# Performance work log

Hardware: AMD Instinct MI355X
Metric: run time of the kernel (lower is better)

## Reference

```python
import jax, jax.numpy as jnp
import numpy as np

B, N, T = 64, 1024, 512  # batch, node_num (= input_dim = hidden_dim), seq_len


def setup_inputs() -> dict:
    key = jax.random.key(0)
    k0, k1, k2, k3, k4 = jax.random.split(key, 5)
    flow_x = jax.random.normal(k0, (B, N, T, 1), dtype=jnp.float32)
    s = 1.0 / np.sqrt(N)  # torch nn.Linear default init bound
    W1 = jax.random.uniform(k1, (N, 2 * N), jnp.float32, -s, s)
    b1 = jax.random.uniform(k2, (2 * N,), jnp.float32, -s, s)
    W2 = jax.random.uniform(k3, (N, N), jnp.float32, -s, s)
    b2 = jax.random.uniform(k4, (N,), jnp.float32, -s, s)
    return {"flow_x": flow_x, "W1": W1, "b1": b1, "W2": W2, "b2": b2}


def reference(flow_x, W1, b1, W2, b2):
    Bs, Nn, Ts, _ = flow_x.shape
    # [B, N, T, 1] -> [B, T, N]
    x = jnp.transpose(flow_x, (0, 2, 1, 3)).reshape(Bs, Ts, Nn)
    # Precompute input projections for all timesteps (batched GEMM)
    xp = x @ W1 + b1                      # [B, T, 2N]
    xh = x @ W2 + b2                      # [B, T, N]
    x1, x2 = jnp.split(xp, 2, axis=-1)    # each [B, T, N]

    def step(h, inp):
        x1t, x2t, xht = inp               # each [B, N]
        hp = h @ W1 + b1                  # [B, 2N]
        h1, h2 = jnp.split(hp, 2, axis=-1)
        z = jax.nn.sigmoid(x1t + h1)
        r = jax.nn.sigmoid(x2t + h2)
        h_hat = jnp.tanh(xht + r * (h @ W2 + b2))
        h_new = z * h + (1.0 - z) * h_hat
        return h_new, None

    h0 = jnp.zeros((Bs, Nn), dtype=x.dtype)
    xs = (jnp.swapaxes(x1, 0, 1), jnp.swapaxes(x2, 0, 1), jnp.swapaxes(xh, 0, 1))
    hT, _ = jax.lax.scan(step, h0, xs)
    # original returns last output reshaped to [B, N, 1, 1]
    return hT.reshape(Bs, Nn, 1, 1)
```

## Files before the change

kernel.cpp:

```cpp
#include <hip/hip_runtime.h>


#define BATCH 64
#define NN 1024
#define TSTEPS 512
#define HB_ELEMS ((size_t)BATCH * NN)
#define SPIN_CAP 16384

typedef __attribute__((ext_vector_type(8))) short short8;
typedef __attribute__((ext_vector_type(8))) unsigned short u16x8;
typedef __attribute__((ext_vector_type(4))) unsigned short u16x4;
typedef __attribute__((ext_vector_type(4))) float f32x4;

#define MFMA16(a, b, c) __builtin_amdgcn_mfma_f32_16x16x32_bf16((a), (b), (c), 0, 0, 0)

__device__ __forceinline__ unsigned short f2bf(float x) {
  union { float f; unsigned u; } v; v.f = x;
  unsigned u = v.u + 0x7FFFu + ((v.u >> 16) & 1u);
  return (unsigned short)(u >> 16);
}
__device__ __forceinline__ float bf2f(unsigned short h) {
  union { unsigned u; float f; } v; v.u = ((unsigned)h) << 16; return v.f;
}

__global__ void trans_x(const float* __restrict__ fx, unsigned short* __restrict__ xT) {
  int bid = blockIdx.x;
  int b   = bid >> 7;
  int rem = bid & 127;
  int kt  = rem >> 3;
  int tt  = rem & 7;
  __shared__ float tl[64][65];
  int tx = threadIdx.x & 63;
  int ty = threadIdx.x >> 6;
  const float* src = fx + ((size_t)(b * NN + kt * 64)) * TSTEPS + tt * 64;
#pragma unroll
  for (int i = 0; i < 16; i++) {
    int kr = i * 4 + ty;
    tl[kr][tx] = src[(size_t)kr * TSTEPS + tx];
  }
  __syncthreads();
#pragma unroll
  for (int i = 0; i < 16; i++) {
    int tr = i * 4 + ty;
    xT[((size_t)((tt * 64 + tr) * 64 + b)) * NN + kt * 64 + tx] = f2bf(tl[tx][tr]);
  }
}

__global__ void prep_w(const float* __restrict__ W1, const float* __restrict__ W2,
                       unsigned short* __restrict__ wt) {
  int bid = blockIdx.x;
  int s    = bid >> 8;
  int tile = bid & 255;
  int kt = tile >> 4, jt = tile & 15;
  const float* src = (s < 2) ? W1 : W2;
  int ld = (s < 2) ? 2048 : 1024;
  int co = (s == 1) ? 1024 : 0;
  __shared__ float tl[64][65];
  int tx = threadIdx.x & 63, ty = threadIdx.x >> 6;
#pragma unroll
  for (int i = 0; i < 16; i++) {
    int kr = i * 4 + ty;
    tl[kr][tx] = src[(size_t)(kt * 64 + kr) * ld + co + jt * 64 + tx];
  }
  __syncthreads();
#pragma unroll
  for (int i = 0; i < 16; i++) {
    int jr = i * 4 + ty;
    wt[((size_t)(s * NN + jt * 64 + jr)) * NN + kt * 64 + tx] = f2bf(tl[tx][jr]);
  }
}

__global__ __launch_bounds__(256) void precompute(
    const unsigned short* __restrict__ xT, const unsigned short* __restrict__ wt,
    const float* __restrict__ b1, const float* __restrict__ b2,
    unsigned short* __restrict__ P2) {
  int m0 = (blockIdx.x / 24) * 128;
  int n0 = (blockIdx.x % 24) * 128;
  __shared__ unsigned short As[128 * 40];
  __shared__ unsigned short Bs[128 * 40];
  int tid = threadIdx.x;
  int wave = tid >> 6, lane = tid & 63, q = lane >> 4, li = lane & 15;
  int wm = wave >> 1, wn = wave & 1;
  f32x4 acc[4][4];
#pragma unroll
  for (int a = 0; a < 4; a++)
#pragma unroll
    for (int b = 0; b < 4; b++) acc[a][b] = (f32x4)(0.f);

  for (int kk = 0; kk < 32; ++kk) {
    int K0 = kk * 32;
#pragma unroll
    for (int e = 0; e < 2; e++) {
      int c = tid * 2 + e;
      int row = c >> 2, part = c & 3;
      *(u16x8*)&As[row * 40 + part * 8] =
          *(const u16x8*)&xT[(size_t)(m0 + row) * NN + K0 + part * 8];
      *(u16x8*)&Bs[row * 40 + part * 8] =
          *(const u16x8*)&wt[(size_t)(n0 + row) * NN + K0 + part * 8];
    }
    __syncthreads();
    short8 af[4], bfr[4];
#pragma unroll
    for (int mt = 0; mt < 4; mt++)
      af[mt] = *(const short8*)&As[(wm * 64 + mt * 16 + li) * 40 + q * 8];
#pragma unroll
    for (int nt = 0; nt < 4; nt++)
      bfr[nt] = *(const short8*)&Bs[(wn * 64 + nt * 16 + li) * 40 + q * 8];
#pragma unroll
    for (int mt = 0; mt < 4; mt++)
#pragma unroll
      for (int nt = 0; nt < 4; nt++)
        acc[mt][nt] = MFMA16(af[mt], bfr[nt], acc[mt][nt]);
    __syncthreads();
  }
#pragma unroll
  for (int mt = 0; mt < 4; mt++) {
    int m = m0 + wm * 64 + mt * 16 + q * 4;
    int t = m >> 6, b = m & 63;
#pragma unroll
    for (int nt = 0; nt < 4; nt++) {
      int n = n0 + wn * 64 + nt * 16 + li;
      float bias = (n < 2048) ? b1[n] : b2[n - 2048];
      int s = n >> 10, j = n & 1023;
      f32x4 a = acc[mt][nt];
      u16x4 pk;
      pk.x = f2bf(a.x + bias); pk.y = f2bf(a.y + bias);
      pk.z = f2bf(a.z + bias); pk.w = f2bf(a.w + bias);
      *(u16x4*)&P2[(((size_t)t * 3 + s) * NN + j) * 64 + b] = pk;
    }
  }
}

#define AL(p)    __hip_atomic_load((p),  __ATOMIC_RELAXED, __HIP_MEMORY_SCOPE_AGENT)
#define AS(p, v) __hip_atomic_store((p), (v), __ATOMIC_RELAXED, __HIP_MEMORY_SCOPE_AGENT)

__global__ __launch_bounds__(256, 1) void gru_scan(
    unsigned short* __restrict__ hb, const unsigned short* __restrict__ wt,
    const unsigned short* __restrict__ P2,
    const float* __restrict__ b1, const float* __restrict__ b2,
    float* __restrict__ out, unsigned* __restrict__ flags) {
  int bid = blockIdx.x;
  int jt = bid & 63, mq = bid >> 6;
  int j0 = jt * 16, m0 = mq * 16;
  int tid = threadIdx.x, wave = tid >> 6, lane = tid & 63, q = lane >> 4, li = lane & 15;
  int kb = wave * 256;

  const short8* Bz = (const short8*)&wt[((size_t)(0 * NN + j0 + li)) * NN + kb + q * 8];
  const short8* Br = (const short8*)&wt[((size_t)(1 * NN + j0 + li)) * NN + kb + q * 8];
  const short8* Bv = (const short8*)&wt[((size_t)(2 * NN + j0 + li)) * NN + kb + q * 8];
  short8 wz[8], wr[8], wv[8];
#pragma unroll
  for (int r = 0; r < 8; r++) {
    wz[r] = Bz[r * 4];
    wr[r] = Br[r * 4];
    wv[r] = Bv[r * 4];
  }

  int j = j0 + li;
  int bbase = m0 + q * 4;
  float b1z = b1[j], b1r = b1[NN + j], b2v = b2[j];
  const unsigned short* pz = &P2[((size_t)0 * NN + j) * 64 + bbase];
  const unsigned short* pr = &P2[((size_t)1 * NN + j) * 64 + bbase];
  const unsigned short* pv = &P2[((size_t)2 * NN + j) * 64 + bbase];
  const size_t pstride = (size_t)3 * NN * 64;

  unsigned* myflag = &flags[(mq * 4 + (jt >> 4)) * 64 + (jt & 15)];
  const unsigned* pollp = &flags[(mq * 4 + wave) * 64 + li];

  const size_t aoff = (size_t)(m0 + li) * 256 + wave * 64 + q * 2;

  f32x4 hc = (f32x4)(0.f);
  __shared__ f32x4 red[2][9][64];

  for (int t = 0; t < TSTEPS; t++) {
    u16x4 pz4, pr4, pv4;
    if (wave == 0) {
      pz4 = *(const u16x4*)pz;
      pr4 = *(const u16x4*)pr;
      pv4 = *(const u16x4*)pv;
    }
    if (t > 0) {
      unsigned tgt = (unsigned)t;
      int spins = 0;
      while (!__all((int)(AL(pollp) >= tgt))) {
        if (++spins > SPIN_CAP) break;
        __builtin_amdgcn_s_sleep(1);
      }
    }
    const unsigned long long* hin =
        (const unsigned long long*)(hb + ((size_t)(t & 3)) * HB_ELEMS);
    union { unsigned long long u[2]; short8 s; } fa[8];
#pragma unroll
    for (int r = 0; r < 8; r++) {
      fa[r].u[0] = AL(hin + aoff + r * 8);
      fa[r].u[1] = AL(hin + aoff + r * 8 + 1);
    }
    f32x4 az = (f32x4)(0.f), ar = (f32x4)(0.f), av = (f32x4)(0.f);
#pragma unroll
    for (int r = 0; r < 8; r++) {
      az = MFMA16(fa[r].s, wz[r], az);
      ar = MFMA16(fa[r].s, wr[r], ar);
      av = MFMA16(fa[r].s, wv[r], av);
    }
    f32x4* rp = &red[t & 1][0][0];
    if (wave > 0) {
      rp[((wave - 1) * 3 + 0) * 64 + lane] = az;
      rp[((wave - 1) * 3 + 1) * 64 + lane] = ar;
      rp[((wave - 1) * 3 + 2) * 64 + lane] = av;
    }
    __syncthreads();
    if (wave == 0) {
#pragma unroll
      for (int w = 0; w < 3; w++) {
        az += rp[(w * 3 + 0) * 64 + lane];
        ar += rp[(w * 3 + 1) * 64 + lane];
        av += rp[(w * 3 + 2) * 64 + lane];
      }
#pragma unroll
      for (int reg = 0; reg < 4; reg++) {
        float z = 1.f / (1.f + __expf(-(az[reg] + bf2f(pz4[reg]) + b1z)));
        float r = 1.f / (1.f + __expf(-(ar[reg] + bf2f(pr4[reg]) + b1r)));
        float x = bf2f(pv4[reg]) + r * (av[reg] + b2v);
        float e = __expf(-2.f * fabsf(x));
        float th = (1.f - e) / (1.f + e);
        float hh = (x >= 0.f) ? th : -th;
        hc[reg] = z * hc[reg] + (1.f - z) * hh;
      }
      if (t < TSTEPS - 1) {
        unsigned* hout = (unsigned*)(hb + ((size_t)((t + 1) & 3)) * HB_ELEMS);
#pragma unroll
        for (int reg = 0; reg < 4; reg++) {
          unsigned mine = f2bf(hc[reg]);
          unsigned other = (unsigned)__shfl_xor((int)mine, 1, 64);
          if ((lane & 1) == 0) {
            unsigned packed = mine | (other << 16);
            AS(&hout[(size_t)(bbase + reg) * (NN / 2) + (j >> 1)], packed);
          }
        }
        asm volatile("s_waitcnt vmcnt(0)" ::: "memory");
        if (lane == 0) AS(myflag, (unsigned)(t + 1));
      }
    }
    pz += pstride; pr += pstride; pv += pstride;
  }

  if (wave == 0) {
#pragma unroll
    for (int reg = 0; reg < 4; reg++)
      out[(size_t)(bbase + reg) * NN + j] = hc[reg];
  }
}

extern "C" void kernel_launch(void* const* d_in, const int* in_sizes, int n_in,
                              void* d_out, int out_size, void* d_ws, size_t ws_size,
                              hipStream_t stream) {
  const float* flow_x = (const float*)d_in[0];
  const float* W1 = (const float*)d_in[1];
  const float* b1 = (const float*)d_in[2];
  const float* W2 = (const float*)d_in[3];
  const float* b2 = (const float*)d_in[4];
  float* out = (float*)d_out;
  char* ws = (char*)d_ws;
  size_t off = 0;
  auto take = [&](size_t bytes) -> char* {
    char* p = ws + off;
    off += (bytes + 255) & ~(size_t)255;
    return p;
  };
  unsigned short* wt    = (unsigned short*)take((size_t)3 * 1024 * 1024 * 2);
  unsigned short* xT    = (unsigned short*)take((size_t)32768 * 1024 * 2);
  unsigned short* P2    = (unsigned short*)take((size_t)512 * 3 * 1024 * 64 * 2);
  unsigned short* hb    = (unsigned short*)take((size_t)4 * HB_ELEMS * 2);
  unsigned*       flags = (unsigned*)take((size_t)16 * 64 * 4);

  if (off > ws_size) {
    hipMemsetAsync(d_out, 0, (size_t)out_size * 4, stream);
    return;
  }

  hipMemsetAsync(hb, 0, HB_ELEMS * 2, stream);
  hipMemsetAsync(flags, 0, (size_t)16 * 64 * 4, stream);

  prep_w<<<768, 256, 0, stream>>>(W1, W2, wt);
  trans_x<<<8192, 256, 0, stream>>>(flow_x, xT);
  precompute<<<6144, 256, 0, stream>>>(xT, wt, b1, b2, P2);

  void* args[] = {&hb, &wt, &P2, &b1, &b2, &out, &flags};
  hipLaunchCooperativeKernel((const void*)gru_scan, dim3(256), dim3(256),
                             args, 0, stream);
}
```

Measured before the change: 3.419 ms.

## Replace per-step flag barrier with step-tagged hidden-state words in the GRU scan

The separate flag array and its store/poll handshake are removed. Each bf16 hidden value is now stored in a 32-bit word together with a 16-bit step tag, packed two per 64-bit atomic store. Consumers spin on the hidden data itself until every tag matches the current step. This drops the vmcnt(0) wait before the flag store and the extra poll round trip on the recurrence's critical path, at the cost of doubling hidden-state traffic and repeating the full loads on every spin.

```diff
diff --git a/kernel.cpp b/kernel.cpp
--- a/kernel.cpp
+++ b/kernel.cpp
@@ -4,7 +4,7 @@
 #define BATCH 64
 #define NN 1024
 #define TSTEPS 512
-#define HB_ELEMS ((size_t)BATCH * NN)
+#define SLOT_U64 ((size_t)BATCH * (NN / 2))
 #define SPIN_CAP 16384
 
 typedef __attribute__((ext_vector_type(8))) short short8;
@@ -135,10 +135,10 @@
 #define AS(p, v) __hip_atomic_store((p), (v), __ATOMIC_RELAXED, __HIP_MEMORY_SCOPE_AGENT)
 
 __global__ __launch_bounds__(256, 1) void gru_scan(
-    unsigned short* __restrict__ hb, const unsigned short* __restrict__ wt,
+    unsigned long long* __restrict__ hb, const unsigned short* __restrict__ wt,
     const unsigned short* __restrict__ P2,
     const float* __restrict__ b1, const float* __restrict__ b2,
-    float* __restrict__ out, unsigned* __restrict__ flags) {
+    float* __restrict__ out) {
   int bid = blockIdx.x;
   int jt = bid & 63, mq = bid >> 6;
   int j0 = jt * 16, m0 = mq * 16;
@@ -164,10 +164,7 @@
   const unsigned short* pv = &P2[((size_t)2 * NN + j) * 64 + bbase];
   const size_t pstride = (size_t)3 * NN * 64;
 
-  unsigned* myflag = &flags[(mq * 4 + (jt >> 4)) * 64 + (jt & 15)];
-  const unsigned* pollp = &flags[(mq * 4 + wave) * 64 + li];
-
-  const size_t aoff = (size_t)(m0 + li) * 256 + wave * 64 + q * 2;
+  const size_t aoff = (size_t)(m0 + li) * 512 + wave * 128 + q * 4;
 
   f32x4 hc = (f32x4)(0.f);
   __shared__ f32x4 red[2][9][64];
@@ -179,28 +176,50 @@
       pr4 = *(const u16x4*)pr;
       pv4 = *(const u16x4*)pv;
     }
-    if (t > 0) {
-      unsigned tgt = (unsigned)t;
+    short8 fa[8];
+    if (t == 0) {
+#pragma unroll
+      for (int r = 0; r < 8; r++) fa[r] = (short8)0;
+    } else {
+      unsigned tg = (unsigned)t;
+      const unsigned long long* hin = hb + ((size_t)(t & 3)) * SLOT_U64 + aoff;
+      unsigned long long raw[8][4];
       int spins = 0;
-      while (!__all((int)(AL(pollp) >= tgt))) {
+      while (true) {
+#pragma unroll
+        for (int r = 0; r < 8; r++)
+#pragma unroll
+          for (int m = 0; m < 4; m++)
+            raw[r][m] = AL(hin + (size_t)r * 16 + m);
+        unsigned bad = 0;
+#pragma unroll
+        for (int r = 0; r < 8; r++)
+#pragma unroll
+          for (int m = 0; m < 4; m++)
+            bad |= (((unsigned)raw[r][m] >> 16) ^ tg);
+        if (__all((int)(bad == 0))) break;
         if (++spins > SPIN_CAP) break;
         __builtin_amdgcn_s_sleep(1);
       }
-    }
-    const unsigned long long* hin =
-        (const unsigned long long*)(hb + ((size_t)(t & 3)) * HB_ELEMS);
-    union { unsigned long long u[2]; short8 s; } fa[8];
+#pragma unroll
+      for (int r = 0; r < 8; r++) {
+        union { unsigned p[4]; short8 s; } u_;
+#pragma unroll
+        for (int m = 0; m < 4; m++) {
+          unsigned lo = (unsigned)raw[r][m];
+          unsigned hi = (unsigned)(raw[r][m] >> 32);
+          u_.p[m] = (lo & 0xFFFFu) | (hi << 16);
+        }
+        fa[r] = u_.s;
+      }
+    }
+
+    f32x4 az = (f32x4)(0.f), ar = (f32x4)(0.f), av = (f32x4)(0.f);
 #pragma unroll
     for (int r = 0; r < 8; r++) {
-      fa[r].u[0] = AL(hin + aoff + r * 8);
-      fa[r].u[1] = AL(hin + aoff + r * 8 + 1);
-    }
-    f32x4 az = (f32x4)(0.f), ar = (f32x4)(0.f), av = (f32x4)(0.f);
-#pragma unroll
-    for (int r = 0; r < 8; r++) {
-      az = MFMA16(fa[r].s, wz[r], az);
-      ar = MFMA16(fa[r].s, wr[r], ar);
-      av = MFMA16(fa[r].s, wv[r], av);
+      az = MFMA16(fa[r], wz[r], az);
+      ar = MFMA16(fa[r], wr[r], ar);
+      av = MFMA16(fa[r], wv[r], av);
     }
     f32x4* rp = &red[t & 1][0][0];
     if (wave > 0) {
@@ -227,18 +246,18 @@
         hc[reg] = z * hc[reg] + (1.f - z) * hh;
       }
       if (t < TSTEPS - 1) {
-        unsigned* hout = (unsigned*)(hb + ((size_t)((t + 1) & 3)) * HB_ELEMS);
+        unsigned long long* hout = hb + ((size_t)((t + 1) & 3)) * SLOT_U64;
+        unsigned tg = (unsigned)(t + 1) << 16;
 #pragma unroll
         for (int reg = 0; reg < 4; reg++) {
-          unsigned mine = f2bf(hc[reg]);
+          unsigned mine = (unsigned)f2bf(hc[reg]) | tg;
           unsigned other = (unsigned)__shfl_xor((int)mine, 1, 64);
           if ((lane & 1) == 0) {
-            unsigned packed = mine | (other << 16);
-            AS(&hout[(size_t)(bbase + reg) * (NN / 2) + (j >> 1)], packed);
+            unsigned long long vv = (unsigned long long)mine |
+                                    ((unsigned long long)other << 32);
+            AS(&hout[(size_t)(bbase + reg) * 512 + (j >> 1)], vv);
           }
         }
-        asm volatile("s_waitcnt vmcnt(0)" ::: "memory");
-        if (lane == 0) AS(myflag, (unsigned)(t + 1));
       }
     }
     pz += pstride; pr += pstride; pv += pstride;
@@ -267,25 +286,23 @@
     off += (bytes + 255) & ~(size_t)255;
     return p;
   };
-  unsigned short* wt    = (unsigned short*)take((size_t)3 * 1024 * 1024 * 2);
-  unsigned short* xT    = (unsigned short*)take((size_t)32768 * 1024 * 2);
-  unsigned short* P2    = (unsigned short*)take((size_t)512 * 3 * 1024 * 64 * 2);
-  unsigned short* hb    = (unsigned short*)take((size_t)4 * HB_ELEMS * 2);
-  unsigned*       flags = (unsigned*)take((size_t)16 * 64 * 4);
+  unsigned short*     wt = (unsigned short*)take((size_t)3 * 1024 * 1024 * 2);
+  unsigned short*     xT = (unsigned short*)take((size_t)32768 * 1024 * 2);
+  unsigned short*     P2 = (unsigned short*)take((size_t)512 * 3 * 1024 * 64 * 2);
+  unsigned long long* hb = (unsigned long long*)take((size_t)4 * SLOT_U64 * 8);
 
   if (off > ws_size) {
     hipMemsetAsync(d_out, 0, (size_t)out_size * 4, stream);
     return;
   }
 
-  hipMemsetAsync(hb, 0, HB_ELEMS * 2, stream);
-  hipMemsetAsync(flags, 0, (size_t)16 * 64 * 4, stream);
+  hipMemsetAsync(hb, 0, (size_t)4 * SLOT_U64 * 8, stream);
 
   prep_w<<<768, 256, 0, stream>>>(W1, W2, wt);
   trans_x<<<8192, 256, 0, stream>>>(flow_x, xT);
   precompute<<<6144, 256, 0, stream>>>(xT, wt, b1, b2, P2);
 
-  void* args[] = {&hb, &wt, &P2, &b1, &b2, &out, &flags};
+  void* args[] = {&hb, &wt, &P2, &b1, &b2, &out};
   hipLaunchCooperativeKernel((const void*)gru_scan, dim3(256), dim3(256),
                              args, 0, stream);
 }
```

New measurement: 6.028 ms. +76.3%, slower.

## Process four batch groups per block and prefetch next group's hidden state

Applied to the files above, without the earlier changes.

The recurrent scan now launches 64 blocks instead of 256, and each block loops over the four 16-row batch groups in turn while keeping its weight slice resident. After each group's MFMAs it polls the next group's flags and, if they are ready, loads that hidden-state fragment early, so the wait for other blocks overlaps with the current group's reduction and gate math. This cuts the number of blocks that must synchronise and lets independent batch groups fill the wait time. The cost is four times more serial work per block on a quarter of the CUs.

```diff
diff --git a/kernel.cpp b/kernel.cpp
--- a/kernel.cpp
+++ b/kernel.cpp
@@ -139,9 +139,8 @@
     const unsigned short* __restrict__ P2,
     const float* __restrict__ b1, const float* __restrict__ b2,
     float* __restrict__ out, unsigned* __restrict__ flags) {
-  int bid = blockIdx.x;
-  int jt = bid & 63, mq = bid >> 6;
-  int j0 = jt * 16, m0 = mq * 16;
+  int jt = blockIdx.x;
+  int j0 = jt * 16;
   int tid = threadIdx.x, wave = tid >> 6, lane = tid & 63, q = lane >> 4, li = lane & 15;
   int kb = wave * 256;
 
@@ -157,97 +156,137 @@
   }
 
   int j = j0 + li;
-  int bbase = m0 + q * 4;
   float b1z = b1[j], b1r = b1[NN + j], b2v = b2[j];
-  const unsigned short* pz = &P2[((size_t)0 * NN + j) * 64 + bbase];
-  const unsigned short* pr = &P2[((size_t)1 * NN + j) * 64 + bbase];
-  const unsigned short* pv = &P2[((size_t)2 * NN + j) * 64 + bbase];
+  const unsigned short* pzb = &P2[((size_t)0 * NN + j) * 64 + q * 4];
+  const unsigned short* prb = &P2[((size_t)1 * NN + j) * 64 + q * 4];
+  const unsigned short* pvb = &P2[((size_t)2 * NN + j) * 64 + q * 4];
   const size_t pstride = (size_t)3 * NN * 64;
 
-  unsigned* myflag = &flags[(mq * 4 + (jt >> 4)) * 64 + (jt & 15)];
-  const unsigned* pollp = &flags[(mq * 4 + wave) * 64 + li];
-
-  const size_t aoff = (size_t)(m0 + li) * 256 + wave * 64 + q * 2;
-
-  f32x4 hc = (f32x4)(0.f);
+  const size_t abase = (size_t)li * 256 + (size_t)wave * 64 + q * 2;
+
+  f32x4 hc[4];
+#pragma unroll
+  for (int g = 0; g < 4; g++) hc[g] = (f32x4)(0.f);
   __shared__ f32x4 red[2][9][64];
 
+  short8 fa[8];
+#pragma unroll
+  for (int r = 0; r < 8; r++) fa[r] = (short8)0;
+  int fa_ok = 1;
+
   for (int t = 0; t < TSTEPS; t++) {
-    u16x4 pz4, pr4, pv4;
-    if (wave == 0) {
-      pz4 = *(const u16x4*)pz;
-      pr4 = *(const u16x4*)pr;
-      pv4 = *(const u16x4*)pv;
+#pragma unroll
+    for (int g = 0; g < 4; g++) {
+      u16x4 pz4, pr4, pv4;
+      if (wave == 0) {
+        size_t po = (size_t)t * pstride + g * 16;
+        pz4 = *(const u16x4*)(pzb + po);
+        pr4 = *(const u16x4*)(prb + po);
+        pv4 = *(const u16x4*)(pvb + po);
+      }
+      if (!fa_ok) {
+        const unsigned* pollp = &flags[(unsigned)(g * 4 + wave) * 64 + li];
+        unsigned tgt = (unsigned)t;
+        int spins = 0;
+        while (!__all((int)(AL(pollp) >= tgt))) {
+          if (++spins > SPIN_CAP) break;
+          __builtin_amdgcn_s_sleep(1);
+        }
+        const unsigned long long* hin =
+            (const unsigned long long*)(hb + ((size_t)(t & 3)) * HB_ELEMS) +
+            (size_t)g * 4096 + abase;
+        union { unsigned long long u[2]; short8 s; } u_;
+#pragma unroll
+        for (int r = 0; r < 8; r++) {
+          u_.u[0] = AL(hin + r * 8);
+          u_.u[1] = AL(hin + r * 8 + 1);
+          fa[r] = u_.s;
+        }
+      }
+      f32x4 az = (f32x4)(0.f), ar = (f32x4)(0.f), av = (f32x4)(0.f);
+#pragma unroll
+      for (int r = 0; r < 8; r++) {
+        az = MFMA16(fa[r], wz[r], az);
+        ar = MFMA16(fa[r], wr[r], ar);
+        av = MFMA16(fa[r], wv[r], av);
+      }
+      {
+        int gn = (g + 1) & 3;
+        int tn = (g == 3) ? t + 1 : t;
+        fa_ok = 0;
+        if (tn < TSTEPS) {
+          if (tn == 0) {
+            fa_ok = 1;
+          } else {
+            const unsigned* pollp = &flags[(unsigned)(gn * 4 + wave) * 64 + li];
+            unsigned f = AL(pollp);
+            if (__all((int)(f >= (unsigned)tn))) {
+              const unsigned long long* hin =
+                  (const unsigned long long*)(hb + ((size_t)(tn & 3)) * HB_ELEMS) +
+                  (size_t)gn * 4096 + abase;
+              union { unsigned long long u[2]; short8 s; } u_;
+#pragma unroll
+              for (int r = 0; r < 8; r++) {
+                u_.u[0] = AL(hin + r * 8);
+                u_.u[1] = AL(hin + r * 8 + 1);
+                fa[r] = u_.s;
+              }
+              fa_ok = 1;
+            }
+          }
+        }
+      }
+      f32x4* rp = &red[g & 1][0][0];
+      if (wave > 0) {
+        rp[((wave - 1) * 3 + 0) * 64 + lane] = az;
+        rp[((wave - 1) * 3 + 1) * 64 + lane] = ar;
+        rp[((wave - 1) * 3 + 2) * 64 + lane] = av;
+      }
+      __syncthreads();
+      if (wave == 0) {
+#pragma unroll
+        for (int w = 0; w < 3; w++) {
+          az += rp[(w * 3 + 0) * 64 + lane];
+          ar += rp[(w * 3 + 1) * 64 + lane];
+          av += rp[(w * 3 + 2) * 64 + lane];
+        }
+#pragma unroll
+        for (int reg = 0; reg < 4; reg++) {
+          float z = 1.f / (1.f + __expf(-(az[reg] + bf2f(pz4[reg]) + b1z)));
+          float r = 1.f / (1.f + __expf(-(ar[reg] + bf2f(pr4[reg]) + b1r)));
+          float x = bf2f(pv4[reg]) + r * (av[reg] + b2v);
+          float e = __expf(-2.f * fabsf(x));
+          float th = (1.f - e) / (1.f + e);
+          float hh = (x >= 0.f) ? th : -th;
+          hc[g][reg] = z * hc[g][reg] + (1.f - z) * hh;
+        }
+        if (t < TSTEPS - 1) {
+          unsigned* hout = (unsigned*)(hb + ((size_t)((t + 1) & 3)) * HB_ELEMS);
+          int bbase = g * 16 + q * 4;
+#pragma unroll
+          for (int reg = 0; reg < 4; reg++) {
+            unsigned mine = f2bf(hc[g][reg]);
+            unsigned other = (unsigned)__shfl_xor((int)mine, 1, 64);
+            if ((lane & 1) == 0) {
+              unsigned packed = mine | (other << 16);
+              AS(&hout[(size_t)(bbase + reg) * (NN / 2) + (j >> 1)], packed);
+            }
+          }
+          asm volatile("s_waitcnt vmcnt(0)" ::: "memory");
+          if (lane == 0)
+            AS(&flags[(unsigned)(g * 4 + (jt >> 4)) * 64 + (jt & 15)],
+               (unsigned)(t + 1));
+        }
+      }
     }
-    if (t > 0) {
-      unsigned tgt = (unsigned)t;
-      int spins = 0;
-      while (!__all((int)(AL(pollp) >= tgt))) {
-        if (++spins > SPIN_CAP) break;
-        __builtin_amdgcn_s_sleep(1);
-      }
-    }
-    const unsigned long long* hin =
-        (const unsigned long long*)(hb + ((size_t)(t & 3)) * HB_ELEMS);
-    union { unsigned long long u[2]; short8 s; } fa[8];
-#pragma unroll
-    for (int r = 0; r < 8; r++) {
-      fa[r].u[0] = AL(hin + aoff + r * 8);
-      fa[r].u[1] = AL(hin + aoff + r * 8 + 1);
-    }
-    f32x4 az = (f32x4)(0.f), ar = (f32x4)(0.f), av = (f32x4)(0.f);
-#pragma unroll
-    for (int r = 0; r < 8; r++) {
-      az = MFMA16(fa[r].s, wz[r], az);
-      ar = MFMA16(fa[r].s, wr[r], ar);
-      av = MFMA16(fa[r].s, wv[r], av);
-    }
-    f32x4* rp = &red[t & 1][0][0];
-    if (wave > 0) {
-      rp[((wave - 1) * 3 + 0) * 64 + lane] = az;
-      rp[((wave - 1) * 3 + 1) * 64 + lane] = ar;
-      rp[((wave - 1) * 3 + 2) * 64 + lane] = av;
-    }
-    __syncthreads();
-    if (wave == 0) {
-#pragma unroll
-      for (int w = 0; w < 3; w++) {
-        az += rp[(w * 3 + 0) * 64 + lane];
-        ar += rp[(w * 3 + 1) * 64 + lane];
-        av += rp[(w * 3 + 2) * 64 + lane];
-      }
-#pragma unroll
-      for (int reg = 0; reg < 4; reg++) {
-        float z = 1.f / (1.f + __expf(-(az[reg] + bf2f(pz4[reg]) + b1z)));
-        float r = 1.f / (1.f + __expf(-(ar[reg] + bf2f(pr4[reg]) + b1r)));
-        float x = bf2f(pv4[reg]) + r * (av[reg] + b2v);
-        float e = __expf(-2.f * fabsf(x));
-        float th = (1.f - e) / (1.f + e);
-        float hh = (x >= 0.f) ? th : -th;
-        hc[reg] = z * hc[reg] + (1.f - z) * hh;
-      }
-      if (t < TSTEPS - 1) {
-        unsigned* hout = (unsigned*)(hb + ((size_t)((t + 1) & 3)) * HB_ELEMS);
-#pragma unroll
-        for (int reg = 0; reg < 4; reg++) {
-          unsigned mine = f2bf(hc[reg]);
-          unsigned other = (unsigned)__shfl_xor((int)mine, 1, 64);
-          if ((lane & 1) == 0) {
-            unsigned packed = mine | (other << 16);
-            AS(&hout[(size_t)(bbase + reg) * (NN / 2) + (j >> 1)], packed);
-          }
-        }
-        asm volatile("s_waitcnt vmcnt(0)" ::: "memory");
-        if (lane == 0) AS(myflag, (unsigned)(t + 1));
-      }
-    }
-    pz += pstride; pr += pstride; pv += pstride;
   }
 
   if (wave == 0) {
 #pragma unroll
-    for (int reg = 0; reg < 4; reg++)
-      out[(size_t)(bbase + reg) * NN + j] = hc[reg];
+    for (int g = 0; g < 4; g++)
+#pragma unroll
+      for (int reg = 0; reg < 4; reg++)
+        out[(size_t)(g * 16 + q * 4 + reg) * NN + j] = hc[g][reg];
   }
 }
 
@@ -286,6 +325,6 @@
   precompute<<<6144, 256, 0, stream>>>(xT, wt, b1, b2, P2);
 
   void* args[] = {&hb, &wt, &P2, &b1, &b2, &out, &flags};
-  hipLaunchCooperativeKernel((const void*)gru_scan, dim3(256), dim3(256),
+  hipLaunchCooperativeKernel((const void*)gru_scan, dim3(64), dim3(256),
                              args, 0, stream);
 }
```

Result: slower. 7.664 ms (+124.2%).
